# Kernel tuning notes

Hardware: AMD Instinct MI355X
Metric: run time of the kernel (lower is better)

## Reference

```python
import jax, jax.numpy as jnp
import numpy as np


def _forward(q, k, Wq, bq, Wk, bk, Wp, bp, eps=1e-4):
    b, ck, hk, wk, dk = k.shape
    n = hk * wk * dk                      # k sequence length == per-block q tokens
    # k branch: flatten spatial, project 256 -> 32
    kf = jnp.einsum('bci,cd->bid', k.reshape(b, ck, n), Wk) + bk   # (b, n, C)
    k_norm = jnp.linalg.norm(kf, axis=1)                           # (b, C): norm over positions (torch dim=1)
    c = q.shape[1]
    hq, wq, dq = q.shape[2], q.shape[3], q.shape[4]
    Nq = hq * wq * dq
    qf = jnp.einsum('bci,cd->bid', q.reshape(b, c, Nq), Wq) + bq   # (b, Nq, C)
    C = qf.shape[-1]
    Bh, Bw, Bd = hq // hk, wq // wk, dq // dk
    G = Bh * Bw * Bd
    # gather all (h_k, w_k, d_k) blocks: (b, G, n, C) -- replaces triple python loop
    qb = (qf.reshape(b, Bh, hk, Bw, wk, Bd, dk, C)
            .transpose(0, 1, 3, 5, 2, 4, 6, 7)
            .reshape(b, G, n, C))
    q_norm = jnp.linalg.norm(qb, axis=2)                           # (b, G, C): per-channel norm over block positions
    denom = jnp.einsum('bc,bgc->bg', k_norm, q_norm) + eps         # scalar per (batch, block)
    # sim[b,g,j,i] = <kf[b,i,:], qb[b,g,j,:]> / denom  (already in post-permute layout)
    sim = jnp.einsum('bic,bgjc->bgji', kf, qb) / denom[:, :, None, None]
    att = jax.nn.softmax(sim, axis=-1)                             # softmax over k positions i
    out = jnp.einsum('bgji,bgic->bgjc', att, qb)                   # (b, G, n, C)
    # min-max renorm over positions within each block (torch dim=1 of (b,n,C))
    mn = out.min(axis=2, keepdims=True)
    mx = out.max(axis=2, keepdims=True)
    v = (out - mn) / (mx - mn + eps)
    # faithful torch reshape: (b, C, n) row-major reinterpreted as (b, hk, wk, dk, C)
    v = v.transpose(0, 1, 3, 2).reshape(b, Bh, Bw, Bd, hk, wk, dk, C)
    # scatter blocks back to full volume
    v = v.transpose(0, 1, 4, 2, 5, 3, 6, 7).reshape(b, hq, wq, dq, C)
    out = jnp.einsum('bhwdc,ce->bhwde', v, Wp) + bp
    return out.transpose(0, 4, 1, 2, 3)                            # (b, C, hq, wq, dq)


def setup_inputs() -> dict:
    key = jax.random.key(0)
    ks = jax.random.split(key, 8)
    nf = 16
    q = jax.random.normal(ks[0], (2, nf * 2, 32, 32, 32), jnp.float32)
    k = jax.random.normal(ks[1], (2, nf * 16, 8, 8, 8), jnp.float32)
    Wq = jax.random.normal(ks[2], (nf * 2, nf * 2), jnp.float32) * 0.05
    bq = jax.random.normal(ks[3], (nf * 2,), jnp.float32) * 0.05
    Wk = jax.random.normal(ks[4], (nf * 16, nf * 2), jnp.float32) * 0.05
    bk = jax.random.normal(ks[5], (nf * 2,), jnp.float32) * 0.05
    Wp = jax.random.normal(ks[6], (nf * 2, nf * 2), jnp.float32) * 0.05
    bp = jax.random.normal(ks[7], (nf * 2,), jnp.float32) * 0.05
    return {"q": q, "k": k, "Wq": Wq, "bq": bq, "Wk": Wk, "bk": bk, "Wp": Wp, "bp": bp}


def reference(q, k, Wq, bq, Wk, bk, Wp, bp):
    return _forward(q, k, Wq, bq, Wk, bk, Wp, bp)
```

## Files before the change

### kernel.cpp

```cpp
#include <hip/hip_runtime.h>
#include <hip/hip_bf16.h>
#include <cstdint>

typedef __attribute__((ext_vector_type(8))) short bf16x8;
typedef __attribute__((ext_vector_type(4))) float f32x4;

static __device__ __forceinline__ float lo16(uint32_t u){ return __uint_as_float(u << 16); }
static __device__ __forceinline__ float hi16(uint32_t u){ return __uint_as_float(u & 0xffff0000u); }
static __device__ __forceinline__ uint32_t f2bf(float x){
    uint32_t u = __float_as_uint(x);
    return (u + 0x7fffu + ((u >> 16) & 1u)) >> 16;
}
static __device__ __forceinline__ uint32_t pack2(float a, float b){
    return f2bf(a) | (f2bf(b) << 16);
}
static __device__ __forceinline__ uint32_t cvtpk(float a, float b){
    uint32_t r;
    asm("v_cvt_pk_bf16_f32 %0, %1, %2" : "=v"(r) : "v"(a), "v"(b));
    return r;
}
static __device__ __forceinline__ void pl32swap(uint32_t &x, uint32_t &y){
    asm("v_permlane32_swap_b32 %0, %1" : "+v"(x), "+v"(y));
}
static __device__ __forceinline__ void pl16swap(uint32_t &x, uint32_t &y){
    asm("v_permlane16_swap_b32 %0, %1" : "+v"(x), "+v"(y));
}

__global__ __launch_bounds__(1024) void k_pre(const float* __restrict__ q,
    const float* __restrict__ k,
    const float* __restrict__ Wq, const float* __restrict__ bq,
    const float* __restrict__ Wk, const float* __restrict__ bk,
    uint32_t* __restrict__ qb_pack, uint32_t* __restrict__ kf_pack)
{
    __shared__ float buf[9248];
    int t = threadIdx.x;
    int blk = blockIdx.x;
    if (blk < 256){
        float* Wq_s = buf;
        float* bq_s = buf + 1024;
        float* q_s  = buf + 1056;
        int bg = blk >> 1, h = blk & 1;
        int b = bg >> 6, g = bg & 63;
        int bh = g >> 4, bw = (g >> 2) & 3, bd = g & 3;
        Wq_s[t] = Wq[t];
        if (t < 32) bq_s[t] = bq[t];
        const float* qbase = q + (size_t)b * 1048576;
        #pragma unroll
        for (int m = 0; m < 2; ++m){
            int L4 = m*1024 + t;
            int f4 = L4 & 1, iw = (L4 >> 1) & 7, ihl = (L4 >> 4) & 3, c = L4 >> 6;
            const float* src = qbase + c*32768 + (bh*8 + h*4 + ihl)*1024
                             + (bw*8 + iw)*32 + bd*8 + f4*4;
            float4 v = *(const float4*)src;
            *(float4*)&q_s[c*256 + ihl*64 + iw*8 + f4*4] = v;
        }
        __syncthreads();
        int d = t & 31, sub = t >> 5;
        float wq[32];
        #pragma unroll
        for (int c = 0; c < 32; ++c) wq[c] = Wq_s[c*32 + d];
        uint32_t* qb_out = qb_pack + (size_t)bg * 8192 + h*4096;
        #pragma unroll
        for (int it = 0; it < 2; ++it){
            int jl = it*128 + sub*4;
            float bb = bq_s[d];
            float a0 = bb, a1 = bb, a2 = bb, a3 = bb;
            #pragma unroll
            for (int c = 0; c < 32; ++c){
                float4 qv = *(const float4*)&q_s[c*256 + jl];
                a0 += qv.x * wq[c];
                a1 += qv.y * wq[c];
                a2 += qv.z * wq[c];
                a3 += qv.w * wq[c];
            }
            float b0 = __shfl_xor(a0, 1, 64), b1 = __shfl_xor(a1, 1, 64);
            float b2 = __shfl_xor(a2, 1, 64), b3 = __shfl_xor(a3, 1, 64);
            if ((d & 1) == 0){
                int w0 = d >> 1;
                qb_out[(jl+0)*16 + w0] = pack2(a0, b0);
                qb_out[(jl+1)*16 + w0] = pack2(a1, b1);
                qb_out[(jl+2)*16 + w0] = pack2(a2, b2);
                qb_out[(jl+3)*16 + w0] = pack2(a3, b3);
            }
        }
    } else {
        float* Wk_s = buf;
        float* bk_s = buf + 8192;
        float* red  = buf + 8224;
        for (int L = t; L < 8192; L += 1024) Wk_s[L] = Wk[L];
        if (t < 32) bk_s[t] = bk[t];
        __syncthreads();
        int kb_blk = blk - 256;
        int b = kb_blk >> 7, i0 = (kb_blk & 127) * 4;
        int d = t & 31, sub = t >> 5;
        int i = i0 + (sub >> 3);
        int cp = sub & 7;
        const float* kbp = k + (size_t)b * 131072;
        float acc = 0.f;
        #pragma unroll 8
        for (int cc = 0; cc < 32; ++cc){
            int c = cp*32 + cc;
            acc += kbp[c*512 + i] * Wk_s[c*32 + d];
        }
        red[sub*32 + d] = acc;
        __syncthreads();
        if (t < 128){
            int isel = t >> 5, dd = t & 31;
            float s = bk_s[dd];
            #pragma unroll
            for (int cp2 = 0; cp2 < 8; ++cp2) s += red[(isel*8 + cp2)*32 + dd];
            float sO = __shfl_xor(s, 1, 64);
            if ((dd & 1) == 0)
                kf_pack[(b*512 + i0 + isel)*16 + (dd >> 1)] = pack2(s, sO);
        }
    }
}

__global__ __launch_bounds__(512) void k_attn_mfma(const uint32_t* __restrict__ kf_pack,
    const uint32_t* __restrict__ qb_pack,
    float* __restrict__ oraw, float* __restrict__ mnp, float* __restrict__ mxp)
{
    __shared__ uint32_t kfs32[8192];
    __shared__ uint16_t qbV16[16384];
    __shared__ float mred[8][64];
    __shared__ float stat[32][32];
    __shared__ float knsh[32], vssh[32], dsh[32];
    __shared__ float denom_s;
    int t = threadIdx.x;
    int blk = blockIdx.x;
    int bg = blk >> 2, jq = blk & 3;
    int b = bg >> 6;
    {
        const uint32_t* src = kf_pack + b*8192;
        #pragma unroll
        for (int m = 0; m < 16; ++m){
            int flat = m*512 + t;
            uint32_t v = src[flat];
            int i = flat >> 4, dp = flat & 15;
            kfs32[i*16 + (((dp>>2) ^ (i&3)) & 3)*4 + (dp&3)] = v;
        }
    }
    {
        const uint32_t* src = qb_pack + (size_t)bg*8192;
        #pragma unroll
        for (int m = 0; m < 16; ++m){
            int flat = m*512 + t;
            int i = flat >> 4, dp = flat & 15;
            uint32_t v = src[flat];
            int d0 = 2*dp, d1 = 2*dp + 1;
            qbV16[d0*512 + (((i>>3) ^ (d0&7)) & 63)*8 + (i&7)] = (uint16_t)(v & 0xffffu);
            qbV16[d1*512 + (((i>>3) ^ (d1&7)) & 63)*8 + (i&7)] = (uint16_t)(v >> 16);
        }
    }
    __syncthreads();
    {
        int dp = t & 15, ig = t >> 4;
        float lo2 = 0.f, hi2 = 0.f;
        #pragma unroll
        for (int ii = 0; ii < 16; ++ii){
            int i = ig*16 + ii;
            uint32_t u = kfs32[i*16 + (((dp>>2) ^ (i&3)) & 3)*4 + (dp&3)];
            float a = lo16(u), c = hi16(u);
            lo2 += a*a; hi2 += c*c;
        }
        stat[ig][dp*2] = lo2; stat[ig][dp*2+1] = hi2;
    }
    __syncthreads();
    if (t < 32){
        float s = 0.f;
        #pragma unroll
        for (int u = 0; u < 32; ++u) s += stat[u][t];
        knsh[t] = s;
    }
    __syncthreads();
    {
        int d = t & 31, ig = t >> 5;
        float q2 = 0.f, vs = 0.f;
        #pragma unroll
        for (int ii = 0; ii < 32; ii += 2){
            int i = ig*32 + ii;
            uint32_t u = *(__shared__ uint32_t*)&qbV16[d*512 + (((i>>3) ^ (d&7)) & 63)*8 + (i&7)];
            float a = lo16(u), c = hi16(u);
            q2 += a*a + c*c; vs += a + c;
        }
        stat[ig][d] = q2; stat[16 + ig][d] = vs;
    }
    __syncthreads();
    if (t < 32){
        float q2 = 0.f, vs = 0.f;
        #pragma unroll
        for (int u = 0; u < 16; ++u){ q2 += stat[u][t]; vs += stat[16+u][t]; }
        vssh[t] = vs;
        dsh[t] = sqrtf(knsh[t]) * sqrtf(q2);
    }
    __syncthreads();
    if (t == 0){
        float s = 0.f;
        #pragma unroll
        for (int d2 = 0; d2 < 32; ++d2) s += dsh[d2];
        denom_s = s + 1e-4f;
    }
    __syncthreads();
    float rden = 1.0f / denom_s;
    int wave = t >> 6, lane = t & 63;
    int ln15 = lane & 15, quad = lane >> 4;
    float vs0[4], vs1[4];
    #pragma unroll
    for (int r = 0; r < 4; ++r){
        vs0[r] = vssh[quad*4 + r];
        vs1[r] = vssh[16 + quad*4 + r];
    }
    float* obase = oraw + (size_t)bg * 16384;
    int jloc = jq*128 + wave*16 + ln15;
    union { bf16x8 v; uint16_t u[8]; } afr;
    #pragma unroll
    for (int jj = 0; jj < 8; ++jj){
        int d = quad*8 + jj;
        afr.u[jj] = qbV16[d*512 + (((jloc>>3) ^ (d&7)) & 63)*8 + (jloc&7)];
    }
    f32x4 pv0 = {0.f,0.f,0.f,0.f}, pv1 = {0.f,0.f,0.f,0.f};
    float pdn = 0.f;
    for (int sb = 0; sb < 4; ++sb){
        #pragma unroll
        for (int ch = 0; ch < 4; ++ch){
            int ib = sb*128 + ch*32;
            int i0 = ib + ln15;
            int i1 = i0 + 16;
            bf16x8 k0 = *(__shared__ bf16x8*)&kfs32[i0*16 + ((quad ^ (i0&3)) & 3)*4];
            bf16x8 k1 = *(__shared__ bf16x8*)&kfs32[i1*16 + ((quad ^ (i1&3)) & 3)*4];
            f32x4 z = {0.f,0.f,0.f,0.f};
            f32x4 s0 = __builtin_amdgcn_mfma_f32_16x16x32_bf16(k0, afr.v, z, 0, 0, 0);
            f32x4 s1 = __builtin_amdgcn_mfma_f32_16x16x32_bf16(k1, afr.v, z, 0, 0, 0);
            float e0[4], e1[4];
            #pragma unroll
            for (int r = 0; r < 4; ++r){
                float x = s0[r] * rden;
                e0[r] = x + x*x*(0.5f + x*(1.0f/6.0f));
                pdn += e0[r];
                x = s1[r] * rden;
                e1[r] = x + x*x*(0.5f + x*(1.0f/6.0f));
                pdn += e1[r];
            }
            uint32_t A0 = cvtpk(e0[0], e0[1]);
            uint32_t A1 = cvtpk(e0[2], e0[3]);
            uint32_t B0 = cvtpk(e1[0], e1[1]);
            uint32_t B1 = cvtpk(e1[2], e1[3]);
            pl32swap(A0, B0); pl16swap(A0, B0);
            pl32swap(A1, B1); pl16swap(A1, B1);
            union { bf16x8 v; uint32_t w[4]; } bp;
            bp.w[0] = A0; bp.w[1] = A1; bp.w[2] = B0; bp.w[3] = B1;
            int ig = ib + quad*8;
            int c0 = ln15, c1 = 16 + ln15;
            bf16x8 av0 = *(__shared__ bf16x8*)&qbV16[c0*512 + (((ig>>3) ^ (c0&7)) & 63)*8];
            bf16x8 av1 = *(__shared__ bf16x8*)&qbV16[c1*512 + (((ig>>3) ^ (c1&7)) & 63)*8];
            pv0 = __builtin_amdgcn_mfma_f32_16x16x32_bf16(av0, bp.v, pv0, 0, 0, 0);
            pv1 = __builtin_amdgcn_mfma_f32_16x16x32_bf16(av1, bp.v, pv1, 0, 0, 0);
        }
    }
    pdn += __shfl_xor(pdn, 16, 64);
    pdn += __shfl_xor(pdn, 32, 64);
    float rl = 1.0f / (512.f + pdn);
    float o0[4], o1[4];
    #pragma unroll
    for (int r = 0; r < 4; ++r){
        o0[r] = (vs0[r] + pv0[r]) * rl;
        o1[r] = (vs1[r] + pv1[r]) * rl;
        obase[(quad*4 + r)*512 + jloc]      = o0[r];
        obase[(16 + quad*4 + r)*512 + jloc] = o1[r];
    }
    #pragma unroll
    for (int r = 0; r < 4; ++r){
        float mnA = o0[r], mxA = o0[r], mnB = o1[r], mxB = o1[r];
        #pragma unroll
        for (int off = 1; off < 16; off <<= 1){
            mnA = fminf(mnA, __shfl_xor(mnA, off, 64));
            mxA = fmaxf(mxA, __shfl_xor(mxA, off, 64));
            mnB = fminf(mnB, __shfl_xor(mnB, off, 64));
            mxB = fmaxf(mxB, __shfl_xor(mxB, off, 64));
        }
        if (ln15 == 0){
            mred[wave][quad*4 + r]      = mnA;
            mred[wave][32 + quad*4 + r] = mxA;
            mred[wave][16 + quad*4 + r] = mnB;
            mred[wave][48 + quad*4 + r] = mxB;
        }
    }
    __syncthreads();
    if (t < 32){
        float mn = 3e38f, mx = -3e38f;
        #pragma unroll
        for (int w = 0; w < 8; ++w){
            mn = fminf(mn, mred[w][t]);
            mx = fmaxf(mx, mred[w][32 + t]);
        }
        int slot = (bg*4 + jq)*32 + t;
        mnp[slot] = mn;
        mxp[slot] = mx;
    }
}

__global__ __launch_bounds__(256) void k_proj(const float* __restrict__ oraw,
    const float* __restrict__ mnp, const float* __restrict__ mxp,
    const float* __restrict__ Wp, const float* __restrict__ bp,
    float* __restrict__ out)
{
    __shared__ float Wp_s[1024], bp_s[32];
    __shared__ float sh_v[32][32];
    __shared__ float sh_o[32][33];
    int t = threadIdx.x;
    if (t < 32) bp_s[t] = bp[t];
    for (int L = t; L < 1024; L += 256) Wp_s[L] = Wp[L];
    int blk = blockIdx.x;
    int b = blk >> 10, p0 = (blk & 1023) * 32;
    int c = t & 31, ip0 = t >> 5;
    float vv[4];
    #pragma unroll
    for (int m = 0; m < 4; ++m){
        int p = p0 + m*8 + ip0;
        int h = p >> 10, w = (p >> 5) & 31, dsp = p & 31;
        int f = (h >> 3)*262144 + (w >> 3)*65536 + (dsp >> 3)*16384
              + (h & 7)*2048 + (w & 7)*256 + (dsp & 7)*32;
        int flat = f + c;
        int cidx = b*2048 + (flat >> 9);
        int s0 = ((cidx >> 5) << 7) + (cidx & 31);
        float o  = oraw[(size_t)b*1048576 + flat];
        float mn = fminf(fminf(mnp[s0], mnp[s0 + 32]), fminf(mnp[s0 + 64], mnp[s0 + 96]));
        float mx = fmaxf(fmaxf(mxp[s0], mxp[s0 + 32]), fmaxf(mxp[s0 + 64], mxp[s0 + 96]));
        vv[m] = (o - mn) / (mx - mn + 1e-4f);
    }
    __syncthreads();
    #pragma unroll
    for (int m = 0; m < 4; ++m) sh_v[m*8 + ip0][c] = vv[m];
    __syncthreads();
    #pragma unroll
    for (int m = 0; m < 4; ++m){
        int pos = m*8 + ip0;
        float acc = bp_s[c];
        #pragma unroll
        for (int cc = 0; cc < 32; ++cc)
            acc += sh_v[pos][cc] * Wp_s[cc*32 + c];
        sh_o[pos][c] = acc;
    }
    __syncthreads();
    #pragma unroll
    for (int m = 0; m < 4; ++m){
        int e = m*8 + (t >> 5), pi = t & 31;
        out[((size_t)(b*32 + e) << 15) + p0 + pi] = sh_o[pi][e];
    }
}

extern "C" void kernel_launch(void* const* d_in, const int* in_sizes, int n_in,
                              void* d_out, int out_size, void* d_ws, size_t ws_size,
                              hipStream_t stream)
{
    const float* q  = (const float*)d_in[0];
    const float* k  = (const float*)d_in[1];
    const float* Wq = (const float*)d_in[2];
    const float* bq = (const float*)d_in[3];
    const float* Wk = (const float*)d_in[4];
    const float* bk = (const float*)d_in[5];
    const float* Wp = (const float*)d_in[6];
    const float* bp = (const float*)d_in[7];

    float* base      = (float*)d_ws;
    uint32_t* kf_pack = (uint32_t*)base;
    uint32_t* qb_pack = (uint32_t*)(base + 16384);
    float* oraw      = base + 1064960;
    float* mnp       = base + 3162112;
    float* mxp       = base + 3178496;
    float* outp      = (float*)d_out;

    hipLaunchKernelGGL(k_pre,       dim3(512),  dim3(1024), 0, stream, q, k, Wq, bq, Wk, bk, qb_pack, kf_pack);
    hipLaunchKernelGGL(k_attn_mfma, dim3(512),  dim3(512),  0, stream, kf_pack, qb_pack, oraw, mnp, mxp);
    hipLaunchKernelGGL(k_proj,      dim3(2048), dim3(256),  0, stream, oraw, mnp, mxp, Wp, bp, outp);
}
```

Measured before the change: 110.2 us.

## Write pre-swizzled LDS images in k_pre and bulk-load them via global_load_lds

k_pre now writes kf and qb directly in the swizzled shared-memory layouts that k_attn_mfma uses, so the attention kernel can copy them into LDS with 16-byte global_load_lds transfers instead of scalar loads and 16-bit scattered stores. The statistics reductions are merged into fewer barriers, and the final denominator sum uses wave shuffles instead of an extra single-thread pass. The sh_v tile in k_proj is padded to reduce bank conflicts. The cost moves to scattered stores in k_pre, and the change depends on the layout contract between the two kernels staying in sync.

```diff
diff --git a/kernel.cpp b/kernel.cpp
--- a/kernel.cpp
+++ b/kernel.cpp
@@ -25,12 +25,17 @@
 static __device__ __forceinline__ void pl16swap(uint32_t &x, uint32_t &y){
     asm("v_permlane16_swap_b32 %0, %1" : "+v"(x), "+v"(y));
 }
+typedef const __attribute__((address_space(1))) uint32_t* gas_u32p;
+typedef __attribute__((address_space(3))) uint32_t* las_u32p;
+static __device__ __forceinline__ void gload_lds16(const uint32_t* g, uint32_t* l){
+    __builtin_amdgcn_global_load_lds((gas_u32p)g, (las_u32p)l, 16, 0, 0);
+}
 
 __global__ __launch_bounds__(1024) void k_pre(const float* __restrict__ q,
     const float* __restrict__ k,
     const float* __restrict__ Wq, const float* __restrict__ bq,
     const float* __restrict__ Wk, const float* __restrict__ bk,
-    uint32_t* __restrict__ qb_pack, uint32_t* __restrict__ kf_pack)
+    uint32_t* __restrict__ qb_img, uint32_t* __restrict__ kf_img)
 {
     __shared__ float buf[9248];
     int t = threadIdx.x;
@@ -42,7 +47,7 @@
         int bg = blk >> 1, h = blk & 1;
         int b = bg >> 6, g = bg & 63;
         int bh = g >> 4, bw = (g >> 2) & 3, bd = g & 3;
-        Wq_s[t] = Wq[t];
+        Wq_s[t & 1023] = Wq[t & 1023];
         if (t < 32) bq_s[t] = bq[t];
         const float* qbase = q + (size_t)b * 1048576;
         #pragma unroll
@@ -59,7 +64,7 @@
         float wq[32];
         #pragma unroll
         for (int c = 0; c < 32; ++c) wq[c] = Wq_s[c*32 + d];
-        uint32_t* qb_out = qb_pack + (size_t)bg * 8192 + h*4096;
+        uint32_t* qb_out = qb_img + (size_t)bg * 8192;
         #pragma unroll
         for (int it = 0; it < 2; ++it){
             int jl = it*128 + sub*4;
@@ -73,15 +78,13 @@
                 a2 += qv.z * wq[c];
                 a3 += qv.w * wq[c];
             }
-            float b0 = __shfl_xor(a0, 1, 64), b1 = __shfl_xor(a1, 1, 64);
-            float b2 = __shfl_xor(a2, 1, 64), b3 = __shfl_xor(a3, 1, 64);
-            if ((d & 1) == 0){
-                int w0 = d >> 1;
-                qb_out[(jl+0)*16 + w0] = pack2(a0, b0);
-                qb_out[(jl+1)*16 + w0] = pack2(a1, b1);
-                qb_out[(jl+2)*16 + w0] = pack2(a2, b2);
-                qb_out[(jl+3)*16 + w0] = pack2(a3, b3);
-            }
+            int jg = h*256 + jl;
+            int grp = ((jg >> 3) ^ (d & 7)) & 63;
+            int word = (jg & 7) >> 1;
+            uint2 wv;
+            wv.x = pack2(a0, a1);
+            wv.y = pack2(a2, a3);
+            *(uint2*)&qb_out[d*256 + grp*4 + word] = wv;
         }
     } else {
         float* Wk_s = buf;
@@ -110,46 +113,45 @@
             #pragma unroll
             for (int cp2 = 0; cp2 < 8; ++cp2) s += red[(isel*8 + cp2)*32 + dd];
             float sO = __shfl_xor(s, 1, 64);
-            if ((dd & 1) == 0)
-                kf_pack[(b*512 + i0 + isel)*16 + (dd >> 1)] = pack2(s, sO);
-        }
-    }
-}
-
-__global__ __launch_bounds__(512) void k_attn_mfma(const uint32_t* __restrict__ kf_pack,
-    const uint32_t* __restrict__ qb_pack,
+            if ((dd & 1) == 0){
+                int dp = dd >> 1;
+                int ii = i0 + isel;
+                kf_img[b*8192 + ii*16 + (((dp>>2) ^ (ii&3)) & 3)*4 + (dp&3)] = pack2(s, sO);
+            }
+        }
+    }
+}
+
+__global__ __launch_bounds__(512) void k_attn_mfma(const uint32_t* __restrict__ kf_img,
+    const uint32_t* __restrict__ qb_img,
     float* __restrict__ oraw, float* __restrict__ mnp, float* __restrict__ mxp)
 {
     __shared__ uint32_t kfs32[8192];
     __shared__ uint16_t qbV16[16384];
+    __shared__ float statA[32][32];
+    __shared__ float statB[16][32];
+    __shared__ float statC[16][32];
     __shared__ float mred[8][64];
-    __shared__ float stat[32][32];
-    __shared__ float knsh[32], vssh[32], dsh[32];
+    __shared__ float vssh[32];
     __shared__ float denom_s;
     int t = threadIdx.x;
     int blk = blockIdx.x;
     int bg = blk >> 2, jq = blk & 3;
     int b = bg >> 6;
+    int wave = t >> 6, lane = t & 63;
     {
-        const uint32_t* src = kf_pack + b*8192;
-        #pragma unroll
-        for (int m = 0; m < 16; ++m){
-            int flat = m*512 + t;
-            uint32_t v = src[flat];
-            int i = flat >> 4, dp = flat & 15;
-            kfs32[i*16 + (((dp>>2) ^ (i&3)) & 3)*4 + (dp&3)] = v;
-        }
-    }
-    {
-        const uint32_t* src = qb_pack + (size_t)bg*8192;
-        #pragma unroll
-        for (int m = 0; m < 16; ++m){
-            int flat = m*512 + t;
-            int i = flat >> 4, dp = flat & 15;
-            uint32_t v = src[flat];
-            int d0 = 2*dp, d1 = 2*dp + 1;
-            qbV16[d0*512 + (((i>>3) ^ (d0&7)) & 63)*8 + (i&7)] = (uint16_t)(v & 0xffffu);
-            qbV16[d1*512 + (((i>>3) ^ (d1&7)) & 63)*8 + (i&7)] = (uint16_t)(v >> 16);
+        const uint32_t* gk = kf_img + b*8192;
+        const uint32_t* gq = qb_img + (size_t)bg*8192;
+        uint32_t* lq = (uint32_t*)qbV16;
+        #pragma unroll
+        for (int m = 0; m < 4; ++m){
+            int off = wave*1024 + m*256;
+            gload_lds16(gk + off + lane*4, kfs32 + off);
+        }
+        #pragma unroll
+        for (int m = 0; m < 4; ++m){
+            int off = wave*1024 + m*256;
+            gload_lds16(gq + off + lane*4, lq + off);
         }
     }
     __syncthreads();
@@ -163,16 +165,8 @@
             float a = lo16(u), c = hi16(u);
             lo2 += a*a; hi2 += c*c;
         }
-        stat[ig][dp*2] = lo2; stat[ig][dp*2+1] = hi2;
-    }
-    __syncthreads();
-    if (t < 32){
-        float s = 0.f;
-        #pragma unroll
-        for (int u = 0; u < 32; ++u) s += stat[u][t];
-        knsh[t] = s;
-    }
-    __syncthreads();
+        statA[ig][dp*2] = lo2; statA[ig][dp*2+1] = hi2;
+    }
     {
         int d = t & 31, ig = t >> 5;
         float q2 = 0.f, vs = 0.f;
@@ -183,26 +177,27 @@
             float a = lo16(u), c = hi16(u);
             q2 += a*a + c*c; vs += a + c;
         }
-        stat[ig][d] = q2; stat[16 + ig][d] = vs;
+        statB[ig][d] = q2; statC[ig][d] = vs;
     }
     __syncthreads();
     if (t < 32){
+        float kn = 0.f;
+        #pragma unroll
+        for (int u = 0; u < 32; ++u) kn += statA[u][t];
         float q2 = 0.f, vs = 0.f;
         #pragma unroll
-        for (int u = 0; u < 16; ++u){ q2 += stat[u][t]; vs += stat[16+u][t]; }
+        for (int u = 0; u < 16; ++u){ q2 += statB[u][t]; vs += statC[u][t]; }
         vssh[t] = vs;
-        dsh[t] = sqrtf(knsh[t]) * sqrtf(q2);
-    }
-    __syncthreads();
-    if (t == 0){
-        float s = 0.f;
-        #pragma unroll
-        for (int d2 = 0; d2 < 32; ++d2) s += dsh[d2];
-        denom_s = s + 1e-4f;
+        float dv = sqrtf(kn) * sqrtf(q2);
+        dv += __shfl_xor(dv, 1, 64);
+        dv += __shfl_xor(dv, 2, 64);
+        dv += __shfl_xor(dv, 4, 64);
+        dv += __shfl_xor(dv, 8, 64);
+        dv += __shfl_xor(dv, 16, 64);
+        if (t == 0) denom_s = dv + 1e-4f;
     }
     __syncthreads();
     float rden = 1.0f / denom_s;
-    int wave = t >> 6, lane = t & 63;
     int ln15 = lane & 15, quad = lane >> 4;
     float vs0[4], vs1[4];
     #pragma unroll
@@ -305,7 +300,7 @@
     float* __restrict__ out)
 {
     __shared__ float Wp_s[1024], bp_s[32];
-    __shared__ float sh_v[32][32];
+    __shared__ float sh_v[32][33];
     __shared__ float sh_o[32][33];
     int t = threadIdx.x;
     if (t < 32) bp_s[t] = bp[t];
@@ -363,14 +358,14 @@
     const float* bp = (const float*)d_in[7];
 
     float* base      = (float*)d_ws;
-    uint32_t* kf_pack = (uint32_t*)base;
-    uint32_t* qb_pack = (uint32_t*)(base + 16384);
+    uint32_t* kf_img = (uint32_t*)base;
+    uint32_t* qb_img = (uint32_t*)(base + 16384);
     float* oraw      = base + 1064960;
     float* mnp       = base + 3162112;
     float* mxp       = base + 3178496;
     float* outp      = (float*)d_out;
 
-    hipLaunchKernelGGL(k_pre,       dim3(512),  dim3(1024), 0, stream, q, k, Wq, bq, Wk, bk, qb_pack, kf_pack);
-    hipLaunchKernelGGL(k_attn_mfma, dim3(512),  dim3(512),  0, stream, kf_pack, qb_pack, oraw, mnp, mxp);
+    hipLaunchKernelGGL(k_pre,       dim3(512),  dim3(1024), 0, stream, q, k, Wq, bq, Wk, bk, qb_img, kf_img);
+    hipLaunchKernelGGL(k_attn_mfma, dim3(512),  dim3(512),  0, stream, kf_img, qb_img, oraw, mnp, mxp);
     hipLaunchKernelGGL(k_proj,      dim3(2048), dim3(256),  0, stream, oraw, mnp, mxp, Wp, bp, outp);
 }
```

Result: slower. 113.1 us (+2.6%).
